# Optimization experiments

Measured on AMD Instinct MI355X. Metric: run time of the kernel, lower is better.

The kernel has to match this reference:

```python
import jax, jax.numpy as jnp
import numpy as np

GROUPS = 32
EPS = 1e-5
NUM_HEADS = 8


def group_norm(x, w, b):
    # x: (B, C, H, W)
    B, C, H, W = x.shape
    xg = x.reshape(B, GROUPS, C // GROUPS, H, W)
    mean = xg.mean(axis=(2, 3, 4), keepdims=True)
    var = xg.var(axis=(2, 3, 4), keepdims=True)
    xg = (xg - mean) * jax.lax.rsqrt(var + EPS)
    x = xg.reshape(B, C, H, W)
    return x * w[None, :, None, None] + b[None, :, None, None]


def setup_inputs() -> dict:
    key = jax.random.key(0)
    ks = jax.random.split(key, 4)
    B, C, H, W = 16, 512, 32, 32
    x = jax.random.normal(ks[0], (B, C, H, W), dtype=jnp.float32)
    gn_w = jnp.ones((C,), dtype=jnp.float32)
    gn_b = jnp.zeros((C,), dtype=jnp.float32)
    qkv_w = jax.random.normal(ks[1], (3 * C, C), dtype=jnp.float32) * 0.02  # 1x1 conv, no bias
    proj_w = jax.random.normal(ks[2], (C, C), dtype=jnp.float32) * 0.02     # 1x1 conv
    proj_b = jax.random.normal(ks[3], (C,), dtype=jnp.float32) * 0.02
    return {"x": x, "gn_w": gn_w, "gn_b": gn_b, "qkv_w": qkv_w,
            "proj_w": proj_w, "proj_b": proj_b}


def reference(x, gn_w, gn_b, qkv_w, proj_w, proj_b):
    B, C, H, W = x.shape
    heads = NUM_HEADS
    head_dim = C // heads
    HW = H * W
    scale = 1.0 / (head_dim ** 0.5)

    x = group_norm(x, gn_w, gn_b)  # residual uses the NORMED x, matching source

    qkv = jnp.einsum('bchw,oc->bohw', x, qkv_w)                     # (B, 3C, H, W)
    qkv = qkv.reshape(B, 3, heads, head_dim, HW)
    q, k, v = qkv[:, 0], qkv[:, 1], qkv[:, 2]                       # (B, heads, head_dim, HW)

    # Replicate the source's exact permute(0,2,3,1)+reshape (scrambles semantics, but faithful)
    def to_bmh(t):
        return jnp.transpose(t, (0, 2, 3, 1)).reshape(B * heads, HW, head_dim)
    q, k, v = to_bmh(q), to_bmh(k), to_bmh(v)

    attn = jax.nn.softmax(jnp.einsum('bnd,bmd->bnm', q, k) * scale, axis=-1)  # (B*heads, HW, HW)
    h = jnp.einsum('bnm,bmd->bnd', attn, v)                                   # (B*heads, HW, head_dim)

    h = h.reshape(B, heads, H, W, head_dim)
    h = jnp.transpose(h, (0, 1, 4, 2, 3)).reshape(B, C, H, W)

    out = jnp.einsum('bchw,oc->bohw', h, proj_w) + proj_b[None, :, None, None]
    return out + x
```

## Files before the change

kernel.cpp:

```cpp
#include <hip/hip_runtime.h>
#include <stdint.h>

typedef unsigned short u16;
typedef short bfrag __attribute__((ext_vector_type(8)));
typedef float ffrag __attribute__((ext_vector_type(4)));
typedef u16 us4 __attribute__((ext_vector_type(4)));
typedef uint32_t u32x4 __attribute__((ext_vector_type(4)));

#define HW 1024
#define C_DIM 512
#define O3 1536
#define BATCH 16

__device__ __forceinline__ u16 f2bf(float f) {
    uint32_t u = __builtin_bit_cast(uint32_t, f);
    u += 0x7FFFu + ((u >> 16) & 1u);
    return (u16)(u >> 16);
}
__device__ __forceinline__ float bf2f(u16 v) {
    return __builtin_bit_cast(float, (uint32_t)v << 16);
}
__device__ __forceinline__ float fexp2(float x) { return __builtin_amdgcn_exp2f(x); }
__device__ __forceinline__ void async16(const u16* src, u16* ldsDst) {
    __builtin_amdgcn_global_load_lds(
        (const __attribute__((address_space(1))) uint32_t*)src,
        (__attribute__((address_space(3))) uint32_t*)ldsDst, 16, 0, 0);
}

__global__ __launch_bounds__(256) void cvt2_kernel(const float* __restrict__ a, u16* __restrict__ da, int n4a,
                                                   const float* __restrict__ b, u16* __restrict__ db, int n4b) {
    int i = blockIdx.x * 256 + threadIdx.x;
    if (i < n4a) {
        float4 v = ((const float4*)a)[i];
        us4 o = { f2bf(v.x), f2bf(v.y), f2bf(v.z), f2bf(v.w) };
        ((us4*)da)[i] = o;
    } else {
        int j = i - n4a;
        if (j < n4b) {
            float4 v = ((const float4*)b)[j];
            us4 o = { f2bf(v.x), f2bf(v.y), f2bf(v.z), f2bf(v.w) };
            ((us4*)db)[j] = o;
        }
    }
}

__global__ __launch_bounds__(256) void groupnorm_kernel(
    const float* __restrict__ x, const float* __restrict__ gw, const float* __restrict__ gb,
    u16* __restrict__ xg, u16* __restrict__ xgt)
{
    __shared__ u16 tile[16 * 1032];
    __shared__ float red[8];
    const int tid = threadIdx.x;
    const int batch = blockIdx.x >> 5, g = blockIdx.x & 31;
    const float* xp = x + ((size_t)batch * C_DIM + g * 16) * HW;

    float s = 0.f, ss = 0.f;
#pragma unroll
    for (int it = 0; it < 16; ++it) {
        int i4 = it * 256 + tid;
        float4 v = ((const float4*)xp)[i4];
        int ci = i4 >> 8;
        int hw = (i4 & 255) * 4;
        s += v.x + v.y + v.z + v.w;
        ss += v.x * v.x + v.y * v.y + v.z * v.z + v.w * v.w;
        us4 u = { f2bf(v.x), f2bf(v.y), f2bf(v.z), f2bf(v.w) };
        *(us4*)&tile[ci * 1032 + hw] = u;
    }
#pragma unroll
    for (int m = 1; m <= 32; m <<= 1) { s += __shfl_xor(s, m, 64); ss += __shfl_xor(ss, m, 64); }
    if ((tid & 63) == 0) { red[tid >> 6] = s; red[4 + (tid >> 6)] = ss; }
    __syncthreads();
    float S = red[0] + red[1] + red[2] + red[3];
    float SS = red[4] + red[5] + red[6] + red[7];
    const float mean = S * (1.f / 16384.f);
    const float istd = rsqrtf(SS * (1.f / 16384.f) - mean * mean + 1e-5f);

    u16* xgp = xg + ((size_t)batch * C_DIM + g * 16) * HW;
#pragma unroll
    for (int it = 0; it < 16; ++it) {
        int i4 = it * 256 + tid;
        int ci = i4 >> 8;
        int hw = (i4 & 255) * 4;
        us4 u = *(us4*)&tile[ci * 1032 + hw];
        float sc = gw[g * 16 + ci] * istd;
        float bi = gb[g * 16 + ci] - mean * sc;
        us4 o = { f2bf(bf2f(u[0]) * sc + bi), f2bf(bf2f(u[1]) * sc + bi),
                  f2bf(bf2f(u[2]) * sc + bi), f2bf(bf2f(u[3]) * sc + bi) };
        *(us4*)&xgp[(size_t)ci * HW + hw] = o;
    }
    u16* xtp = xgt + (size_t)batch * HW * C_DIM + g * 16;
#pragma unroll
    for (int it = 0; it < 16; ++it) {
        int hw = (tid >> 2) + it * 64;
        int c0 = (tid & 3) * 4;
        us4 o;
#pragma unroll
        for (int k2 = 0; k2 < 4; ++k2) {
            int ci = c0 + k2;
            float sc = gw[g * 16 + ci] * istd;
            float bi = gb[g * 16 + ci] - mean * sc;
            o[k2] = f2bf(bf2f(tile[ci * 1032 + hw]) * sc + bi);
        }
        *(us4*)&xtp[(size_t)hw * C_DIM + c0] = o;
    }
}

template<int EPI>
__global__ __launch_bounds__(256) void gemm_kernel(
    const u16* __restrict__ A, const u16* __restrict__ B, void* __restrict__ Out,
    const float* __restrict__ bias, const u16* __restrict__ resid, u16* __restrict__ vtout,
    int Ntiles, int tpb, int ldOut, long aBatch, long bBatch, long oBatch, long rBatch)
{
    __shared__ __align__(16) u16 smem[24576];
    const int tid = threadIdx.x;
    const int l = tid & 63, w = tid >> 6;
    const int nwg = gridDim.x;
    const int swz = (blockIdx.x & 7) * (nwg >> 3) + (blockIdx.x >> 3);
    const int batch = swz / tpb, t = swz % tpb;
    const int tm = t / Ntiles, tn = t % Ntiles;
    A += (size_t)batch * aBatch + (size_t)tm * 128 * 512;
    B += (size_t)batch * bBatch + (size_t)tn * 128 * 512;

    auto stage = [&](const u16* gbase, u16* lds, int kt) {
#pragma unroll
        for (int i = 0; i < 2; ++i) {
            int L = i * 256 + tid;
            int row = L >> 2, cs = L & 3;
            int c = cs ^ ((row & 3) ^ ((row >> 2) & 3));
            async16(gbase + (size_t)row * 512 + kt * 32 + c * 8,
                    lds + (size_t)(i * 256 + (tid & 192)) * 8);
        }
    };

    ffrag acc[4][4] = {};
    stage(A, smem, 0);        stage(B, smem + 12288, 0);
    stage(A, smem + 4096, 1); stage(B, smem + 16384, 1);
    const int wr = (w >> 1) * 64, wc = (w & 1) * 64;
#pragma unroll
    for (int kt = 0; kt < 16; ++kt) {
        const int cur = kt % 3;
        if (kt < 15) asm volatile("s_waitcnt vmcnt(4)" ::: "memory");
        else         asm volatile("s_waitcnt vmcnt(0)" ::: "memory");
        __builtin_amdgcn_s_barrier();
        __builtin_amdgcn_sched_barrier(0);
        if (kt < 14) {
            int nxt = (kt + 2) % 3;
            stage(A, smem + nxt * 4096, kt + 2);
            stage(B, smem + 12288 + nxt * 4096, kt + 2);
        }
        const u16* As = smem + cur * 4096;
        const u16* Bs = smem + 12288 + cur * 4096;
        bfrag a[4], bb[4];
#pragma unroll
        for (int i = 0; i < 4; ++i) {
            int row = wr + i * 16 + (l & 15);
            int ch = (l >> 4) ^ ((row & 3) ^ ((row >> 2) & 3));
            a[i] = *(const bfrag*)&As[row * 32 + ch * 8];
            int col = wc + i * 16 + (l & 15);
            int ch2 = (l >> 4) ^ ((col & 3) ^ ((col >> 2) & 3));
            bb[i] = *(const bfrag*)&Bs[col * 32 + ch2 * 8];
        }
        __builtin_amdgcn_s_setprio(1);
#pragma unroll
        for (int i = 0; i < 4; ++i)
#pragma unroll
            for (int j = 0; j < 4; ++j)
                acc[i][j] = __builtin_amdgcn_mfma_f32_16x16x32_bf16(a[i], bb[j], acc[i][j], 0, 0, 0);
        __builtin_amdgcn_s_setprio(0);
    }
    __syncthreads();
    const int rbase = tm * 128 + wr + ((l >> 4) << 2);
    const int cbase = tn * 128 + wc + (l & 15);
    if (EPI == 0) {
        if (tn >= 8) {
            u16* vb = vtout + (size_t)batch * 8 * 64 * HW;
            const int hd0 = tn * 128 - 1024;
#pragma unroll
            for (int i = 0; i < 4; ++i)
#pragma unroll
                for (int j = 0; j < 4; ++j) {
                    int hd_l = wc + (l & 15) + j * 16;
                    int m_l = wr + i * 16 + ((l >> 4) << 2);
                    int s_l = (m_l & 96) | ((m_l & 12) << 1) | ((m_l & 16) >> 2);
                    int c4 = s_l >> 2;
                    int c4s = c4 ^ (hd_l & 7);
                    us4 pk = { f2bf(acc[i][j][0]), f2bf(acc[i][j][1]),
                               f2bf(acc[i][j][2]), f2bf(acc[i][j][3]) };
                    *(us4*)&smem[hd_l * 128 + c4s * 4] = pk;
                }
            __syncthreads();
#pragma unroll
            for (int it = 0; it < 16; ++it) {
                int f4 = it * 256 + tid;
                int hd_l = f4 >> 5, c4 = f4 & 31;
                int c4s = c4 ^ (hd_l & 7);
                us4 v = *(const us4*)&smem[hd_l * 128 + c4s * 4];
                *(us4*)&vb[(size_t)(hd0 + hd_l) * HW + tm * 128 + c4 * 4] = v;
            }
        } else {
            u16* outp = (u16*)Out + (size_t)batch * oBatch;
#pragma unroll
            for (int i = 0; i < 4; ++i)
#pragma unroll
                for (int j = 0; j < 4; ++j)
#pragma unroll
                    for (int r = 0; r < 4; ++r)
                        outp[(size_t)(rbase + i * 16 + r) * ldOut + cbase + j * 16] = f2bf(acc[i][j][r]);
        }
    } else {
        float* outp = (float*)Out + (size_t)batch * oBatch;
        const u16* rp = resid + (size_t)batch * rBatch;
#pragma unroll
        for (int i = 0; i < 4; ++i)
#pragma unroll
            for (int j = 0; j < 4; ++j)
#pragma unroll
                for (int r = 0; r < 4; ++r) {
                    int rr = rbase + i * 16 + r, cc = cbase + j * 16;
                    outp[(size_t)rr * ldOut + cc] =
                        acc[i][j][r] + bias[rr] + bf2f(rp[(size_t)rr * ldOut + cc]);
                }
    }
}

__global__ __launch_bounds__(512, 4) void attn_kernel(const u16* __restrict__ qkvt,
                                                      const u16* __restrict__ vt,
                                                      u16* __restrict__ ht)
{
    __shared__ __align__(16) u16 KVs[6 * 4096];
    const int tid = threadIdx.x, l = tid & 63, w = tid >> 6, g = l >> 4;
    const int swz = ((blockIdx.x & 7) << 6) + (blockIdx.x >> 3);
    const int nt = swz & 3, h = (swz >> 2) & 7, batch = swz >> 5;
    const u16* Qb = qkvt + (size_t)batch * HW * O3 + h * 64;
    const u16* Kb = Qb + 512;
    const u16* Vtb = vt + (size_t)(batch * 8 + h) * 64 * HW;
    const int n0 = nt * 256 + w * 32;
    const float cexp = 0.125f * 1.44269504f;

    bfrag qf[2][2];
#pragma unroll
    for (int ni = 0; ni < 2; ++ni)
#pragma unroll
        for (int kc = 0; kc < 2; ++kc)
            qf[ni][kc] = *(const bfrag*)&Qb[(size_t)(n0 + ni * 16 + (l & 15)) * O3 + kc * 32 + g * 8];

    bfrag ones;
#pragma unroll
    for (int k = 0; k < 8; ++k) ones[k] = (short)0x3F80;

    auto stageK = [&](int ms, u16* lds) {
        int row = tid >> 3, c = (tid & 7) ^ (row & 7);
        async16(&Kb[(size_t)(ms * 64 + row) * O3 + c * 8], lds + (size_t)(tid & 448) * 8);
    };
    auto stageV = [&](int ms, u16* lds) {
        int row = tid >> 3, c = (tid & 7) ^ (row & 7);
        async16(&Vtb[(size_t)row * HW + ms * 64 + c * 8], lds + (size_t)(tid & 448) * 8);
    };

    ffrag hacc[2][4] = {};
    ffrag accl[2] = {};

    stageK(0, KVs);        stageV(0, KVs + 3 * 4096);
    stageK(1, KVs + 4096); stageV(1, KVs + 4 * 4096);

#pragma unroll
    for (int ms = 0; ms < 16; ++ms) {
        const int cur = ms % 3;
        const u16* Ksc = KVs + cur * 4096;
        const u16* Vsc = KVs + (3 + cur) * 4096;
        if (ms < 15) asm volatile("s_waitcnt vmcnt(2)" ::: "memory");
        else         asm volatile("s_waitcnt vmcnt(0)" ::: "memory");
        __builtin_amdgcn_s_barrier();
        __builtin_amdgcn_sched_barrier(0);
        if (ms < 14) {
            int nxt = (ms + 2) % 3;
            stageK(ms + 2, KVs + nxt * 4096);
            stageV(ms + 2, KVs + (3 + nxt) * 4096);
        }

        ffrag s[2][4] = {};
        __builtin_amdgcn_s_setprio(1);
#pragma unroll
        for (int mj = 0; mj < 4; ++mj)
#pragma unroll
            for (int kc = 0; kc < 2; ++kc) {
                int m = mj * 16 + (l & 15);
                int ch = (kc * 4 + g) ^ (m & 7);
                bfrag kf = *(const bfrag*)&Ksc[m * 64 + ch * 8];
#pragma unroll
                for (int ni = 0; ni < 2; ++ni)
                    s[ni][mj] = __builtin_amdgcn_mfma_f32_16x16x32_bf16(kf, qf[ni][kc], s[ni][mj], 0, 0, 0);
            }
        __builtin_amdgcn_s_setprio(0);

        u32x4 pk[2][2];
#pragma unroll
        for (int ni = 0; ni < 2; ++ni)
#pragma unroll
            for (int kc = 0; kc < 2; ++kc)
#pragma unroll
                for (int hh = 0; hh < 2; ++hh) {
                    int mj = kc * 2 + hh;
                    float p0 = fexp2(s[ni][mj][0] * cexp);
                    float p1 = fexp2(s[ni][mj][1] * cexp);
                    float p2 = fexp2(s[ni][mj][2] * cexp);
                    float p3 = fexp2(s[ni][mj][3] * cexp);
                    pk[ni][kc][hh * 2] = __builtin_amdgcn_perm(
                        __builtin_bit_cast(uint32_t, p1), __builtin_bit_cast(uint32_t, p0), 0x07060302u);
                    pk[ni][kc][hh * 2 + 1] = __builtin_amdgcn_perm(
                        __builtin_bit_cast(uint32_t, p3), __builtin_bit_cast(uint32_t, p2), 0x07060302u);
                }

        __builtin_amdgcn_s_setprio(1);
#pragma unroll
        for (int kc = 0; kc < 2; ++kc) {
            bfrag pf0 = __builtin_bit_cast(bfrag, pk[0][kc]);
            bfrag pf1 = __builtin_bit_cast(bfrag, pk[1][kc]);
            accl[0] = __builtin_amdgcn_mfma_f32_16x16x32_bf16(pf0, ones, accl[0], 0, 0, 0);
            accl[1] = __builtin_amdgcn_mfma_f32_16x16x32_bf16(pf1, ones, accl[1], 0, 0, 0);
#pragma unroll
            for (int dj = 0; dj < 4; ++dj) {
                int d = dj * 16 + (l & 15);
                int ch = (kc * 4 + g) ^ (d & 7);
                bfrag vf = *(const bfrag*)&Vsc[d * 64 + ch * 8];
                hacc[0][dj] = __builtin_amdgcn_mfma_f32_16x16x32_bf16(pf0, vf, hacc[0][dj], 0, 0, 0);
                hacc[1][dj] = __builtin_amdgcn_mfma_f32_16x16x32_bf16(pf1, vf, hacc[1][dj], 0, 0, 0);
            }
        }
        __builtin_amdgcn_s_setprio(0);
    }

    u16* hp = ht + (size_t)batch * HW * C_DIM + h * 64;
#pragma unroll
    for (int ni = 0; ni < 2; ++ni) {
        float linv[4];
#pragma unroll
        for (int r = 0; r < 4; ++r) linv[r] = __builtin_amdgcn_rcpf(accl[ni][r]);
#pragma unroll
        for (int dj = 0; dj < 4; ++dj)
#pragma unroll
            for (int r = 0; r < 4; ++r) {
                int n = n0 + ni * 16 + g * 4 + r;
                int d = dj * 16 + (l & 15);
                hp[(size_t)n * C_DIM + d] = f2bf(hacc[ni][dj][r] * linv[r]);
            }
    }
}

extern "C" void kernel_launch(void* const* d_in, const int* in_sizes, int n_in,
                              void* d_out, int out_size, void* d_ws, size_t ws_size,
                              hipStream_t stream)
{
    const float* x = (const float*)d_in[0];
    const float* gw = (const float*)d_in[1];
    const float* gb = (const float*)d_in[2];
    const float* qkvw = (const float*)d_in[3];
    const float* projw = (const float*)d_in[4];
    const float* projb = (const float*)d_in[5];
    float* out = (float*)d_out;
    char* ws = (char*)d_ws;
    u16* xg    = (u16*)(ws);
    u16* xgt   = (u16*)(ws + 16777216);
    u16* qkvt  = (u16*)(ws + 33554432);
    u16* vt    = (u16*)(ws + 83886080);
    u16* qkvwb = (u16*)(ws + 100663296);
    u16* projwb= (u16*)(ws + 102236160);
    u16* ht    = xgt;

    cvt2_kernel<<<1024, 256, 0, stream>>>(qkvw, qkvwb, 196608, projw, projwb, 65536);
    groupnorm_kernel<<<512, 256, 0, stream>>>(x, gw, gb, xg, xgt);
    gemm_kernel<0><<<1536, 256, 0, stream>>>(
        xgt, qkvwb, qkvt, nullptr, nullptr, vt, 12, 96, 1536, 524288L, 0L, 1572864L, 0L);
    attn_kernel<<<512, 512, 0, stream>>>(qkvt, vt, ht);
    gemm_kernel<1><<<512, 256, 0, stream>>>(
        projwb, ht, out, projb, xg, nullptr, 8, 32, 1024, 0L, 524288L, 524288L, 524288L);
}
```

Before: 113.4 us.

## Split GEMM into specialized kernels with 256x128 triple-buffered QKV tile

The templated GEMM becomes two kernels. The QKV projection now uses a 256x128 output tile with 8x4 MFMA fragments per wave, triple-buffered LDS staging and 2 waves-per-SIMD launch bounds, halving the grid to 768 blocks. This is meant to raise arithmetic intensity and hide load latency. The V-transpose epilogue is widened to 256 rows with a new XOR swizzle. The projection kernel hardcodes its constants and drops the trailing sync, at the cost of higher register and LDS use per block.

```diff
diff --git a/kernel.cpp b/kernel.cpp
--- a/kernel.cpp
+++ b/kernel.cpp
@@ -105,21 +105,131 @@
     }
 }
 
-template<int EPI>
-__global__ __launch_bounds__(256) void gemm_kernel(
-    const u16* __restrict__ A, const u16* __restrict__ B, void* __restrict__ Out,
-    const float* __restrict__ bias, const u16* __restrict__ resid, u16* __restrict__ vtout,
-    int Ntiles, int tpb, int ldOut, long aBatch, long bBatch, long oBatch, long rBatch)
+__global__ __launch_bounds__(256, 2) void qkv_gemm_kernel(
+    const u16* __restrict__ A, const u16* __restrict__ B, u16* __restrict__ Out,
+    u16* __restrict__ vtout)
+{
+    __shared__ __align__(16) u16 smem[36864];
+    const int tid = threadIdx.x;
+    const int l = tid & 63, w = tid >> 6;
+    const int swz = (blockIdx.x & 7) * 96 + (blockIdx.x >> 3);
+    const int batch = swz / 48, t = swz % 48;
+    const int tm = t / 12, tn = t % 12;
+    A += (size_t)batch * (HW * C_DIM) + (size_t)tm * 256 * 512;
+    B += (size_t)tn * 128 * 512;
+
+    auto stageA = [&](u16* lds, int kt) {
+#pragma unroll
+        for (int i = 0; i < 4; ++i) {
+            int L = i * 256 + tid;
+            int row = L >> 2, cs = L & 3;
+            int c = cs ^ ((row & 3) ^ ((row >> 2) & 3));
+            async16(A + (size_t)row * 512 + kt * 32 + c * 8,
+                    lds + (size_t)(i * 256 + (tid & 192)) * 8);
+        }
+    };
+    auto stageB = [&](u16* lds, int kt) {
+#pragma unroll
+        for (int i = 0; i < 2; ++i) {
+            int L = i * 256 + tid;
+            int row = L >> 2, cs = L & 3;
+            int c = cs ^ ((row & 3) ^ ((row >> 2) & 3));
+            async16(B + (size_t)row * 512 + kt * 32 + c * 8,
+                    lds + (size_t)(i * 256 + (tid & 192)) * 8);
+        }
+    };
+
+    ffrag acc[8][4] = {};
+    stageA(smem, 0);        stageB(smem + 24576, 0);
+    stageA(smem + 8192, 1); stageB(smem + 28672, 1);
+    const int wm = (w >> 1) * 128, wn = (w & 1) * 64;
+#pragma unroll
+    for (int kt = 0; kt < 16; ++kt) {
+        const int cur = kt % 3;
+        if (kt < 15) asm volatile("s_waitcnt vmcnt(6)" ::: "memory");
+        else         asm volatile("s_waitcnt vmcnt(0)" ::: "memory");
+        __builtin_amdgcn_s_barrier();
+        __builtin_amdgcn_sched_barrier(0);
+        if (kt < 14) {
+            int nxt = (kt + 2) % 3;
+            stageA(smem + nxt * 8192, kt + 2);
+            stageB(smem + 24576 + nxt * 4096, kt + 2);
+        }
+        const u16* As = smem + cur * 8192;
+        const u16* Bs = smem + 24576 + cur * 4096;
+        bfrag a[8], bb[4];
+#pragma unroll
+        for (int j = 0; j < 4; ++j) {
+            int col = wn + j * 16 + (l & 15);
+            int ch2 = (l >> 4) ^ ((col & 3) ^ ((col >> 2) & 3));
+            bb[j] = *(const bfrag*)&Bs[col * 32 + ch2 * 8];
+        }
+#pragma unroll
+        for (int i = 0; i < 8; ++i) {
+            int row = wm + i * 16 + (l & 15);
+            int ch = (l >> 4) ^ ((row & 3) ^ ((row >> 2) & 3));
+            a[i] = *(const bfrag*)&As[row * 32 + ch * 8];
+        }
+        __builtin_amdgcn_s_setprio(1);
+#pragma unroll
+        for (int i = 0; i < 8; ++i)
+#pragma unroll
+            for (int j = 0; j < 4; ++j)
+                acc[i][j] = __builtin_amdgcn_mfma_f32_16x16x32_bf16(a[i], bb[j], acc[i][j], 0, 0, 0);
+        __builtin_amdgcn_s_setprio(0);
+    }
+    __syncthreads();
+    const int rbase = tm * 256 + wm + ((l >> 4) << 2);
+    const int cbase = tn * 128 + wn + (l & 15);
+    if (tn < 8) {
+        u16* outp = Out + (size_t)batch * (HW * O3);
+#pragma unroll
+        for (int i = 0; i < 8; ++i)
+#pragma unroll
+            for (int j = 0; j < 4; ++j)
+#pragma unroll
+                for (int r = 0; r < 4; ++r)
+                    outp[(size_t)(rbase + i * 16 + r) * O3 + cbase + j * 16] = f2bf(acc[i][j][r]);
+    } else {
+        u16* vb = vtout + (size_t)batch * 8 * 64 * HW;
+        const int hd0 = tn * 128 - 1024;
+#pragma unroll
+        for (int i = 0; i < 8; ++i)
+#pragma unroll
+            for (int j = 0; j < 4; ++j) {
+                int hd_l = wn + (l & 15) + j * 16;
+                int m_l = wm + i * 16 + ((l >> 4) << 2);
+                int s_l = (m_l & ~31) | ((m_l & 12) << 1) | ((m_l & 16) >> 2) | (m_l & 3);
+                int c4 = s_l >> 2;
+                int c4s = c4 ^ (hd_l & 63);
+                us4 pk = { f2bf(acc[i][j][0]), f2bf(acc[i][j][1]),
+                           f2bf(acc[i][j][2]), f2bf(acc[i][j][3]) };
+                *(us4*)&smem[hd_l * 256 + c4s * 4] = pk;
+            }
+        __syncthreads();
+#pragma unroll
+        for (int it = 0; it < 32; ++it) {
+            int f4 = it * 256 + tid;
+            int hd_l = f4 >> 6, c4 = f4 & 63;
+            int c4s = c4 ^ (hd_l & 63);
+            us4 v = *(const us4*)&smem[hd_l * 256 + c4s * 4];
+            *(us4*)&vb[(size_t)(hd0 + hd_l) * HW + tm * 256 + c4 * 4] = v;
+        }
+    }
+}
+
+__global__ __launch_bounds__(256) void proj_gemm_kernel(
+    const u16* __restrict__ A, const u16* __restrict__ B, float* __restrict__ Out,
+    const float* __restrict__ bias, const u16* __restrict__ resid)
 {
     __shared__ __align__(16) u16 smem[24576];
     const int tid = threadIdx.x;
     const int l = tid & 63, w = tid >> 6;
-    const int nwg = gridDim.x;
-    const int swz = (blockIdx.x & 7) * (nwg >> 3) + (blockIdx.x >> 3);
-    const int batch = swz / tpb, t = swz % tpb;
-    const int tm = t / Ntiles, tn = t % Ntiles;
-    A += (size_t)batch * aBatch + (size_t)tm * 128 * 512;
-    B += (size_t)batch * bBatch + (size_t)tn * 128 * 512;
+    const int swz = (blockIdx.x & 7) * 64 + (blockIdx.x >> 3);
+    const int batch = swz / 32, t = swz % 32;
+    const int tm = t / 8, tn = t % 8;
+    A += (size_t)tm * 128 * 512;
+    B += (size_t)batch * (HW * C_DIM) + (size_t)tn * 128 * 512;
 
     auto stage = [&](const u16* gbase, u16* lds, int kt) {
 #pragma unroll
@@ -168,59 +278,20 @@
                 acc[i][j] = __builtin_amdgcn_mfma_f32_16x16x32_bf16(a[i], bb[j], acc[i][j], 0, 0, 0);
         __builtin_amdgcn_s_setprio(0);
     }
-    __syncthreads();
     const int rbase = tm * 128 + wr + ((l >> 4) << 2);
     const int cbase = tn * 128 + wc + (l & 15);
-    if (EPI == 0) {
-        if (tn >= 8) {
-            u16* vb = vtout + (size_t)batch * 8 * 64 * HW;
-            const int hd0 = tn * 128 - 1024;
-#pragma unroll
-            for (int i = 0; i < 4; ++i)
-#pragma unroll
-                for (int j = 0; j < 4; ++j) {
-                    int hd_l = wc + (l & 15) + j * 16;
-                    int m_l = wr + i * 16 + ((l >> 4) << 2);
-                    int s_l = (m_l & 96) | ((m_l & 12) << 1) | ((m_l & 16) >> 2);
-                    int c4 = s_l >> 2;
-                    int c4s = c4 ^ (hd_l & 7);
-                    us4 pk = { f2bf(acc[i][j][0]), f2bf(acc[i][j][1]),
-                               f2bf(acc[i][j][2]), f2bf(acc[i][j][3]) };
-                    *(us4*)&smem[hd_l * 128 + c4s * 4] = pk;
-                }
-            __syncthreads();
-#pragma unroll
-            for (int it = 0; it < 16; ++it) {
-                int f4 = it * 256 + tid;
-                int hd_l = f4 >> 5, c4 = f4 & 31;
-                int c4s = c4 ^ (hd_l & 7);
-                us4 v = *(const us4*)&smem[hd_l * 128 + c4s * 4];
-                *(us4*)&vb[(size_t)(hd0 + hd_l) * HW + tm * 128 + c4 * 4] = v;
+    float* outp = Out + (size_t)batch * (C_DIM * HW);
+    const u16* rp = resid + (size_t)batch * (C_DIM * HW);
+#pragma unroll
+    for (int i = 0; i < 4; ++i)
+#pragma unroll
+        for (int j = 0; j < 4; ++j)
+#pragma unroll
+            for (int r = 0; r < 4; ++r) {
+                int rr = rbase + i * 16 + r, cc = cbase + j * 16;
+                outp[(size_t)rr * HW + cc] =
+                    acc[i][j][r] + bias[rr] + bf2f(rp[(size_t)rr * HW + cc]);
             }
-        } else {
-            u16* outp = (u16*)Out + (size_t)batch * oBatch;
-#pragma unroll
-            for (int i = 0; i < 4; ++i)
-#pragma unroll
-                for (int j = 0; j < 4; ++j)
-#pragma unroll
-                    for (int r = 0; r < 4; ++r)
-                        outp[(size_t)(rbase + i * 16 + r) * ldOut + cbase + j * 16] = f2bf(acc[i][j][r]);
-        }
-    } else {
-        float* outp = (float*)Out + (size_t)batch * oBatch;
-        const u16* rp = resid + (size_t)batch * rBatch;
-#pragma unroll
-        for (int i = 0; i < 4; ++i)
-#pragma unroll
-            for (int j = 0; j < 4; ++j)
-#pragma unroll
-                for (int r = 0; r < 4; ++r) {
-                    int rr = rbase + i * 16 + r, cc = cbase + j * 16;
-                    outp[(size_t)rr * ldOut + cc] =
-                        acc[i][j][r] + bias[rr] + bf2f(rp[(size_t)rr * ldOut + cc]);
-                }
-    }
 }
 
 __global__ __launch_bounds__(512, 4) void attn_kernel(const u16* __restrict__ qkvt,
@@ -369,9 +440,7 @@
 
     cvt2_kernel<<<1024, 256, 0, stream>>>(qkvw, qkvwb, 196608, projw, projwb, 65536);
     groupnorm_kernel<<<512, 256, 0, stream>>>(x, gw, gb, xg, xgt);
-    gemm_kernel<0><<<1536, 256, 0, stream>>>(
-        xgt, qkvwb, qkvt, nullptr, nullptr, vt, 12, 96, 1536, 524288L, 0L, 1572864L, 0L);
+    qkv_gemm_kernel<<<768, 256, 0, stream>>>(xgt, qkvwb, qkvt, vt);
     attn_kernel<<<512, 512, 0, stream>>>(qkvt, vt, ht);
-    gemm_kernel<1><<<512, 256, 0, stream>>>(
-        projwb, ht, out, projb, xg, nullptr, 8, 32, 1024, 0L, 524288L, 524288L, 524288L);
-}
+    proj_gemm_kernel<<<512, 256, 0, stream>>>(projwb, ht, out, projb, xg);
+}
```

After: 111.1 us. 1.02x faster.
